# Optimization experiments

Measured on AMD Instinct MI355X. Metric: run time of the kernel, lower is better.

Reference implementation:

```python
import jax, jax.numpy as jnp
import numpy as np

B, N, C = 16, 2048, 3           # images, proposals/image, classes (incl. background)
K = 100                         # num_detections kept per class
SCORE_THRESH = 0.05
NMS_THRESH = 0.5
MIN_ANGLE = 10.0                # process_box min width (self.min_angle)
WX, WW = 1.0, 1.0               # box_coder reg_weights
NEG = jnp.float32(-1e9)


def setup_inputs() -> dict:
    key = jax.random.key(0)
    k1, k2, k3, k4 = jax.random.split(key, 4)
    class_logit = jax.random.normal(k1, (B, N, C), jnp.float32)
    box_regression = jax.random.normal(k2, (B, N, 2 * C), jnp.float32) * 0.1
    starts = jax.random.uniform(k3, (B, N), dtype=jnp.float32) * 300.0
    widths = jax.random.uniform(k4, (B, N), dtype=jnp.float32) * 50.0 + 12.0
    proposal = jnp.stack([starts, starts + widths], axis=-1)  # [B,N,2] 1-D intervals
    return {"class_logit": class_logit, "box_regression": box_regression,
            "proposal": proposal, "image_shape": 360}


def _decode(delta, prop):
    w = prop[:, 1] - prop[:, 0]
    ctr = prop[:, 0] + 0.5 * w
    dx = delta[:, 0] / WX
    dw = jnp.minimum(delta[:, 1] / WW, 4.0)  # clamp like torchvision
    pc = dx * w + ctr
    pw = jnp.exp(dw) * w
    return jnp.stack([pc - 0.5 * pw, pc + 0.5 * pw], axis=-1)  # [N,2]


def _iou_1d(a, b):
    inter = jnp.maximum(0.0, jnp.minimum(a[:, None, 1], b[None, :, 1])
                        - jnp.maximum(a[:, None, 0], b[None, :, 0]))
    union = (a[:, None, 1] - a[:, None, 0]) + (b[None, :, 1] - b[None, :, 0]) - inter
    return inter / jnp.maximum(union, 1e-8)  # [Na,Nb]


def _infer_one_class(score, delta, prop, image_shape):
    # score [N], delta [N,2], prop [N,2] -> [K,3] (start, end, score); invalid slots score=NEG
    box = _decode(delta, prop)
    lo = jnp.clip(box[:, 0], 0.0, image_shape)
    hi = jnp.clip(box[:, 1], 0.0, image_shape)
    box = jnp.stack([lo, hi], axis=-1)
    valid = ((hi - lo) >= MIN_ANGLE) & (score >= SCORE_THRESH)
    ms = jnp.where(valid, score, NEG)
    order = jnp.argsort(-ms)
    b = box[order]
    s = ms[order]
    sup = jax.lax.stop_gradient(_iou_1d(b, b)) > NMS_THRESH  # [N,N] bool
    idx = jnp.arange(N)

    def body(keep, i):  # greedy NMS in score order
        kill = sup[i] & keep[i] & (idx > i)
        return keep & ~kill, None

    keep0 = s > 0.5 * NEG
    keep, _ = jax.lax.scan(body, keep0, idx)
    ks = jnp.where(keep, s, NEG)
    top_s, top_i = jax.lax.top_k(ks, K)
    top_b = b[top_i]
    return jnp.concatenate([top_b, top_s[:, None]], axis=-1)  # [K,3]


def reference(class_logit, box_regression, proposal, image_shape):
    img = jnp.float32(image_shape)
    scores = jax.nn.softmax(class_logit, axis=-1)[..., 1:]        # [B,N,C-1] fg classes
    deltas = box_regression.reshape(B, N, C, 2)[:, :, 1:]         # [B,N,C-1,2]
    scores = jnp.moveaxis(scores, -1, 1)                          # [B,C-1,N]
    deltas = jnp.moveaxis(deltas, 2, 1)                           # [B,C-1,N,2]
    f = jax.vmap(jax.vmap(_infer_one_class, in_axes=(0, 0, None, None)),
                 in_axes=(0, 0, 0, None))
    return f(scores, deltas, proposal, img)  # [B, C-1, K, 3]
```

## Files before the change

### kernel.cpp

```cpp
#include <hip/hip_runtime.h>
#include <math.h>

#define B_IMG 16
#define N_PROP 2048
#define C_CLS 3
#define K_OUT 100
#define NTHREADS 1024
#define NWAVES (NTHREADS / 64)

__global__ __launch_bounds__(NTHREADS)
void roiheads_kernel(const float* __restrict__ class_logit,
                     const float* __restrict__ box_reg,
                     const float* __restrict__ proposal,
                     const int* __restrict__ image_shape_p,
                     float* __restrict__ out)
{
#pragma clang fp contract(off)
    __shared__ unsigned long long skey[N_PROP];
    __shared__ float llo[N_PROP], lhi[N_PROP];
    __shared__ float slo[N_PROP], shi[N_PROP];
    __shared__ unsigned char keep[N_PROP];
    __shared__ unsigned short alv[2][N_PROP];
    __shared__ float clo[64], chi[64];
    __shared__ int wsum[NWAVES], woff[NWAVES];
    __shared__ int sh_nvalid, sh_ccnt, sh_nanew;

    const int tid = threadIdx.x;
    const int lane = tid & 63;
    const int wid = tid >> 6;
    const int img = blockIdx.x >> 1;
    const int cls = blockIdx.x & 1;

    int raw = image_shape_p[0];
    float imgf = (raw > 0 && raw < 1000000) ? (float)raw : __int_as_float(raw);

    if (tid == 0) sh_nvalid = 0;

    for (int n = tid; n < N_PROP; n += NTHREADS) {
        const float* lg = class_logit + ((size_t)img * N_PROP + n) * C_CLS;
        float l0 = lg[0], l1 = lg[1], l2 = lg[2];
        float mx = fmaxf(l0, fmaxf(l1, l2));
        float e0 = (float)exp((double)(l0 - mx));
        float e1 = (float)exp((double)(l1 - mx));
        float e2 = (float)exp((double)(l2 - mx));
        float denom = (e0 + e1) + e2;
        float ec = (cls == 0) ? e1 : e2;
        float score = ec / denom;

        const float* dr = box_reg + ((size_t)img * N_PROP + n) * (2 * C_CLS) + 2 * (cls + 1);
        float dx = dr[0];
        float dw = fminf(dr[1], 4.0f);
        const float* pp = proposal + ((size_t)img * N_PROP + n) * 2;
        float p0 = pp[0], p1 = pp[1];
        float w = p1 - p0;
        float ctr = p0 + 0.5f * w;
        float t = dx * w;
        float pc = t + ctr;
        float pw = (float)exp((double)dw) * w;
        float half = 0.5f * pw;
        float lo = pc - half;
        float hi = pc + half;
        lo = fminf(fmaxf(lo, 0.0f), imgf);
        hi = fminf(fmaxf(hi, 0.0f), imgf);
        bool valid = ((hi - lo) >= 10.0f) && (score >= 0.05f);
        float ms = valid ? score : -1e9f;

        llo[n] = lo; lhi[n] = hi;
        unsigned int u = __float_as_uint(ms);
        unsigned int e = (u & 0x80000000u) ? ~u : (u | 0x80000000u);
        skey[n] = ((unsigned long long)e << 32) |
                  (unsigned long long)(0xFFFFFFFFu - (unsigned int)n);
    }
    __syncthreads();

    for (int k = 2; k <= N_PROP; k <<= 1) {
        for (int j = k >> 1; j >= 1; j >>= 1) {
            int i = ((tid & ~(j - 1)) << 1) | (tid & (j - 1));
            int part = i | j;
            unsigned long long a = skey[i], b = skey[part];
            bool desc_blk = ((i & k) == 0);
            bool sw = desc_blk ? (a < b) : (a > b);
            if (sw) { skey[i] = b; skey[part] = a; }
            __syncthreads();
        }
    }

    for (int i = tid; i < N_PROP; i += NTHREADS) {
        unsigned long long kk = skey[i];
        unsigned int e = (unsigned int)(kk >> 32);
        unsigned int sb = (e & 0x80000000u) ? (e & 0x7FFFFFFFu) : ~e;
        float s = __uint_as_float(sb);
        unsigned int n = 0xFFFFFFFFu - (unsigned int)(kk & 0xFFFFFFFFull);
        slo[i] = llo[n];
        shi[i] = lhi[n];
        keep[i] = 0;
        bool v = (s > -5e8f);
        unsigned long long mb = __ballot(v);
        if (lane == 0) atomicAdd(&sh_nvalid, __popcll(mb));
        alv[0][i] = (unsigned short)i;
    }
    __syncthreads();

    int na = sh_nvalid;
    int cur = 0;

    while (na > 0) {
        const int m = (na < 64) ? na : 64;
        if (tid == 64) sh_nanew = 0;
        if (tid < 64) {
            bool inr = (lane < m);
            unsigned short p = inr ? alv[cur][lane] : 0;
            float blo = inr ? slo[p] : 0.0f;
            float bhi = inr ? shi[p] : 0.0f;
            float bw = bhi - blo;
            bool alive = inr;
            unsigned long long msk = __ballot(alive);
            while (msk) {
                int curi = __builtin_ctzll(msk);
                float cl = __shfl(blo, curi, 64);
                float ch = __shfl(bhi, curi, 64);
                if (alive && lane > curi) {
                    float inter = fminf(bhi, ch) - fmaxf(blo, cl);
                    inter = fmaxf(inter, 0.0f);
                    float uni = bw + (ch - cl) - inter;
                    if (inter / fmaxf(uni, 1e-8f) > 0.5f) alive = false;
                }
                msk = __ballot(alive);
                if (curi >= 63) msk = 0;
                else msk &= ~((2ull << curi) - 1ull);
            }
            unsigned long long fm = __ballot(alive);
            if (alive) keep[p] = 1;
            unsigned long long below = (1ull << lane) - 1ull;
            int rank = __popcll(fm & below);
            if (alive) { clo[rank] = blo; chi[rank] = bhi; }
            if (lane == 0) sh_ccnt = __popcll(fm);
        }
        __syncthreads();
        const int cnt = sh_ccnt;

        for (int start = 64; start < na; start += NTHREADS) {
            int t = start + tid;
            unsigned short q = 0;
            bool surv = false;
            if (t < na) {
                q = alv[cur][t];
                float qlo = slo[q], qhi = shi[q];
                float qw = qhi - qlo;
                surv = true;
                for (int r = 0; r < cnt; ++r) {
                    float cl = clo[r], ch = chi[r];
                    float inter = fminf(qhi, ch) - fmaxf(qlo, cl);
                    inter = fmaxf(inter, 0.0f);
                    float uni = qw + (ch - cl) - inter;
                    if (inter / fmaxf(uni, 1e-8f) > 0.5f) { surv = false; break; }
                }
            }
            unsigned long long mb = __ballot(surv);
            if (lane == 0) wsum[wid] = __popcll(mb);
            __syncthreads();
            if (tid == 0) {
                int acc = sh_nanew;
                for (int w2 = 0; w2 < NWAVES; ++w2) { woff[w2] = acc; acc += wsum[w2]; }
                sh_nanew = acc;
            }
            __syncthreads();
            if (surv) {
                unsigned long long below = (1ull << lane) - 1ull;
                alv[cur ^ 1][woff[wid] + __popcll(mb & below)] = q;
            }
            __syncthreads();
        }
        na = sh_nanew;
        cur ^= 1;
    }

    if (tid < 64) {
        int nk = 0;
        for (int blk = 0; blk < N_PROP / 64; ++blk) {
            bool k = keep[blk * 64 + lane] != 0;
            nk += __popcll(__ballot(k));
        }
        float* outp = out + (((size_t)img * 2 + cls) * K_OUT) * 3;
        unsigned long long below = (1ull << lane) - 1ull;
        int kc = 0, nc = 0;
        for (int blk = 0; blk < N_PROP / 64; ++blk) {
            int p = blk * 64 + lane;
            bool k = keep[p] != 0;
            unsigned long long mb = __ballot(k);
            int rk = kc + __popcll(mb & below);
            int rn = nc + __popcll((~mb) & below);
            if (k) {
                if (rk < K_OUT) {
                    unsigned long long kk2 = skey[p];
                    unsigned int e = (unsigned int)(kk2 >> 32);
                    unsigned int sb = (e & 0x80000000u) ? (e & 0x7FFFFFFFu) : ~e;
                    outp[rk * 3 + 0] = slo[p];
                    outp[rk * 3 + 1] = shi[p];
                    outp[rk * 3 + 2] = __uint_as_float(sb);
                }
            } else {
                int oi = nk + rn;
                if (oi < K_OUT) {
                    outp[oi * 3 + 0] = slo[p];
                    outp[oi * 3 + 1] = shi[p];
                    outp[oi * 3 + 2] = -1e9f;
                }
            }
            int pc2 = __popcll(mb);
            kc += pc2;
            nc += 64 - pc2;
        }
    }
}

extern "C" void kernel_launch(void* const* d_in, const int* in_sizes, int n_in,
                              void* d_out, int out_size, void* d_ws, size_t ws_size,
                              hipStream_t stream) {
    const float* class_logit = (const float*)d_in[0];
    const float* box_reg     = (const float*)d_in[1];
    const float* prop        = (const float*)d_in[2];
    const int*   image_shape = (const int*)d_in[3];
    float* out = (float*)d_out;

    roiheads_kernel<<<dim3(B_IMG * 2), dim3(NTHREADS), 0, stream>>>(
        class_logit, box_reg, prop, image_shape, out);
}
```

Measured before the change: 107.3 us.

## Register-resident bitonic sort stages, ballot-mask NMS, parallel output scatter

Each thread now holds two sort keys in registers. Bitonic stages with stride up to 64 run through cross-lane shuffles instead of shared memory and __syncthreads, which leaves only the large-stride passes in LDS. The 64-candidate wave NMS is rewritten around readlane and a ballot-derived alive mask, so it no longer needs a ballot plus shuffle per iteration. The final compaction precomputes per-block keep masks so all waves write output in parallel instead of a single wave scanning serially. The cost is more register pressure and somewhat more complex indexing.

```diff
diff --git a/kernel.cpp b/kernel.cpp
--- a/kernel.cpp
+++ b/kernel.cpp
@@ -7,6 +7,16 @@
 #define K_OUT 100
 #define NTHREADS 1024
 #define NWAVES (NTHREADS / 64)
+#define NBLK64 (N_PROP / 64)
+
+__device__ __forceinline__ unsigned long long shfl_xor_u64(unsigned long long v, int lx) {
+    unsigned int lo = (unsigned int)__shfl_xor((int)(unsigned int)(v & 0xffffffffull), lx, 64);
+    unsigned int hi = (unsigned int)__shfl_xor((int)(unsigned int)(v >> 32), lx, 64);
+    return ((unsigned long long)hi << 32) | (unsigned long long)lo;
+}
+__device__ __forceinline__ float readlane_f(float v, int l) {
+    return __int_as_float(__builtin_amdgcn_readlane(__float_as_int(v), l));
+}
 
 __global__ __launch_bounds__(NTHREADS)
 void roiheads_kernel(const float* __restrict__ class_logit,
@@ -22,6 +32,7 @@
     __shared__ unsigned char keep[N_PROP];
     __shared__ unsigned short alv[2][N_PROP];
     __shared__ float clo[64], chi[64];
+    __shared__ unsigned long long kmask[NBLK64];
     __shared__ int wsum[NWAVES], woff[NWAVES];
     __shared__ int sh_nvalid, sh_ccnt, sh_nanew;
 
@@ -36,7 +47,11 @@
 
     if (tid == 0) sh_nvalid = 0;
 
-    for (int n = tid; n < N_PROP; n += NTHREADS) {
+    const int p0 = (wid << 7) | (lane << 1);
+    const int p1 = p0 | 1;
+
+    auto decode = [&](int n) -> unsigned long long {
+#pragma clang fp contract(off)
         const float* lg = class_logit + ((size_t)img * N_PROP + n) * C_CLS;
         float l0 = lg[0], l1 = lg[1], l2 = lg[2];
         float mx = fmaxf(l0, fmaxf(l1, l2));
@@ -51,9 +66,9 @@
         float dx = dr[0];
         float dw = fminf(dr[1], 4.0f);
         const float* pp = proposal + ((size_t)img * N_PROP + n) * 2;
-        float p0 = pp[0], p1 = pp[1];
-        float w = p1 - p0;
-        float ctr = p0 + 0.5f * w;
+        float pA = pp[0], pB = pp[1];
+        float w = pB - pA;
+        float ctr = pA + 0.5f * w;
         float t = dx * w;
         float pc = t + ctr;
         float pw = (float)exp((double)dw) * w;
@@ -68,13 +83,37 @@
         llo[n] = lo; lhi[n] = hi;
         unsigned int u = __float_as_uint(ms);
         unsigned int e = (u & 0x80000000u) ? ~u : (u | 0x80000000u);
-        skey[n] = ((unsigned long long)e << 32) |
-                  (unsigned long long)(0xFFFFFFFFu - (unsigned int)n);
-    }
-    __syncthreads();
-
-    for (int k = 2; k <= N_PROP; k <<= 1) {
-        for (int j = k >> 1; j >= 1; j >>= 1) {
+        return ((unsigned long long)e << 32) |
+               (unsigned long long)(0xFFFFFFFFu - (unsigned int)n);
+    };
+    unsigned long long r0 = decode(p0);
+    unsigned long long r1 = decode(p1);
+
+    auto pass_inreg = [&](int k, int j) {
+        if (j == 1) {
+            bool desc = ((p0 & k) == 0);
+            bool sw = desc ? (r0 < r1) : (r0 > r1);
+            if (sw) { unsigned long long t = r0; r0 = r1; r1 = t; }
+        } else {
+            int lx = j >> 1;
+            unsigned long long o0 = shfl_xor_u64(r0, lx);
+            unsigned long long o1 = shfl_xor_u64(r1, lx);
+            bool desc = ((p0 & k) == 0);
+            bool lower = ((p0 & j) == 0);
+            bool takeMax = (lower == desc);
+            r0 = takeMax ? (r0 > o0 ? r0 : o0) : (r0 < o0 ? r0 : o0);
+            r1 = takeMax ? (r1 > o1 ? r1 : o1) : (r1 < o1 ? r1 : o1);
+        }
+    };
+
+    for (int k = 2; k <= 128; k <<= 1)
+        for (int j = k >> 1; j >= 1; j >>= 1)
+            pass_inreg(k, j);
+
+    for (int k = 256; k <= N_PROP; k <<= 1) {
+        skey[p0] = r0; skey[p1] = r1;
+        __syncthreads();
+        for (int j = k >> 1; j >= 128; j >>= 1) {
             int i = ((tid & ~(j - 1)) << 1) | (tid & (j - 1));
             int part = i | j;
             unsigned long long a = skey[i], b = skey[part];
@@ -83,7 +122,12 @@
             if (sw) { skey[i] = b; skey[part] = a; }
             __syncthreads();
         }
-    }
+        r0 = skey[p0]; r1 = skey[p1];
+        for (int j = 64; j >= 1; j >>= 1)
+            pass_inreg(k, j);
+    }
+    skey[p0] = r0; skey[p1] = r1;
+    __syncthreads();
 
     for (int i = tid; i < N_PROP; i += NTHREADS) {
         unsigned long long kk = skey[i];
@@ -109,32 +153,28 @@
         if (tid == 64) sh_nanew = 0;
         if (tid < 64) {
             bool inr = (lane < m);
-            unsigned short p = inr ? alv[cur][lane] : 0;
+            unsigned short p = inr ? alv[cur][lane] : (unsigned short)0;
             float blo = inr ? slo[p] : 0.0f;
             float bhi = inr ? shi[p] : 0.0f;
             float bw = bhi - blo;
-            bool alive = inr;
-            unsigned long long msk = __ballot(alive);
-            while (msk) {
-                int curi = __builtin_ctzll(msk);
-                float cl = __shfl(blo, curi, 64);
-                float ch = __shfl(bhi, curi, 64);
-                if (alive && lane > curi) {
-                    float inter = fminf(bhi, ch) - fmaxf(blo, cl);
-                    inter = fmaxf(inter, 0.0f);
-                    float uni = bw + (ch - cl) - inter;
-                    if (inter / fmaxf(uni, 1e-8f) > 0.5f) alive = false;
-                }
-                msk = __ballot(alive);
-                if (curi >= 63) msk = 0;
-                else msk &= ~((2ull << curi) - 1ull);
-            }
-            unsigned long long fm = __ballot(alive);
+            unsigned long long A = (m >= 64) ? ~0ull : ((1ull << m) - 1ull);
+            unsigned long long kept = 0;
+            while (A) {
+                int c = __builtin_ctzll(A);
+                float cl = readlane_f(blo, c);
+                float ch = readlane_f(bhi, c);
+                float inter = fmaxf(fminf(bhi, ch) - fmaxf(blo, cl), 0.0f);
+                float uni = bw + (ch - cl) - inter;
+                bool kill = (lane > c) && (inter / fmaxf(uni, 1e-8f) > 0.5f);
+                unsigned long long row = __ballot(kill);
+                kept |= (1ull << c);
+                A &= ~(row | (1ull << c));
+            }
+            bool alive = inr && ((kept >> lane) & 1ull);
             if (alive) keep[p] = 1;
-            unsigned long long below = (1ull << lane) - 1ull;
-            int rank = __popcll(fm & below);
+            int rank = __popcll(kept & ((1ull << lane) - 1ull));
             if (alive) { clo[rank] = blo; chi[rank] = bhi; }
-            if (lane == 0) sh_ccnt = __popcll(fm);
+            if (lane == 0) sh_ccnt = __popcll(kept);
         }
         __syncthreads();
         const int cnt = sh_ccnt;
@@ -175,19 +215,26 @@
         cur ^= 1;
     }
 
-    if (tid < 64) {
-        int nk = 0;
-        for (int blk = 0; blk < N_PROP / 64; ++blk) {
-            bool k = keep[blk * 64 + lane] != 0;
-            nk += __popcll(__ballot(k));
-        }
+    for (int blk = wid; blk < NBLK64; blk += NWAVES) {
+        bool kk = keep[blk * 64 + lane] != 0;
+        unsigned long long mb = __ballot(kk);
+        if (lane == 0) kmask[blk] = mb;
+    }
+    __syncthreads();
+    {
         float* outp = out + (((size_t)img * 2 + cls) * K_OUT) * 3;
         unsigned long long below = (1ull << lane) - 1ull;
-        int kc = 0, nc = 0;
-        for (int blk = 0; blk < N_PROP / 64; ++blk) {
+        for (int blk = wid; blk < NBLK64; blk += NWAVES) {
+            int kc = 0, nc = 0, nk = 0;
+            for (int b = 0; b < NBLK64; ++b) {
+                int pc = __popcll(kmask[b]);
+                nk += pc;
+                if (b < blk) { kc += pc; nc += 64 - pc; }
+            }
+            if (kc >= K_OUT && nk + nc >= K_OUT && nc >= K_OUT) continue;
             int p = blk * 64 + lane;
-            bool k = keep[p] != 0;
-            unsigned long long mb = __ballot(k);
+            unsigned long long mb = kmask[blk];
+            bool k = (mb >> lane) & 1ull;
             int rk = kc + __popcll(mb & below);
             int rn = nc + __popcll((~mb) & below);
             if (k) {
@@ -207,9 +254,6 @@
                     outp[oi * 3 + 2] = -1e9f;
                 }
             }
-            int pc2 = __popcll(mb);
-            kc += pc2;
-            nc += 64 - pc2;
         }
     }
 }
```

Result: faster. 99.42 us (-7.3%).
